# Kernel optimization log

Hardware: AMD Instinct MI355X
Metric: run time of the kernel (lower is better)

Reference implementation:

```python
import jax, jax.numpy as jnp
import numpy as np

B, S, D, H, DH = 2, 2048, 768, 12, 64
GAMMA = 0.5
SMOOTHING = 1.0  # softmax_attn_smoothing scalar (non-trainable weight in the original)
SCALE = 1.0 / float(np.sqrt(DH))


def setup_inputs() -> dict:
    key = jax.random.key(0)
    ks = jax.random.split(key, 8)
    w = 0.02
    return {
        "inp": jax.random.normal(ks[0], (B, S, D), dtype=jnp.float32),
        "pos_emb": jax.random.normal(ks[1], (S, D), dtype=jnp.float32),
        "Wq_inp": jax.random.normal(ks[2], (D, H * DH), dtype=jnp.float32) * w,
        "Wk_inp": jax.random.normal(ks[3], (D, H * DH), dtype=jnp.float32) * w,
        "Wq_pos": jax.random.normal(ks[4], (D, H * DH), dtype=jnp.float32) * w,
        "Wk_pos": jax.random.normal(ks[5], (D, H * DH), dtype=jnp.float32) * w,
        "Wv": jax.random.normal(ks[6], (D, H * DH), dtype=jnp.float32) * w,
        "Wo": jax.random.normal(ks[7], (H * DH, D), dtype=jnp.float32) * w,
    }


def reference(inp, pos_emb, Wq_inp, Wk_inp, Wq_pos, Wk_pos, Wv, Wo):
    # projections; note original reshape order: [..., d_head, n_head]
    q_i = (inp @ Wq_inp).reshape(B, S, DH, H)
    k_i = (inp @ Wk_inp).reshape(B, S, DH, H)
    q_p = (pos_emb @ Wq_pos).reshape(S, DH, H)
    k_p = (pos_emb @ Wk_pos).reshape(S, DH, H)
    v = (inp @ Wv).reshape(B, S, DH, H)

    # content-content stream: [B,S,S,H], softmax over key axis (axis=2)
    score_inp = jnp.einsum("bidh,bjdh->bijh", q_i, k_i) * (SCALE * SMOOTHING)
    prob_inp = jax.nn.softmax(score_inp, axis=2)

    # position-position stream: [S,S,H], softmax over key axis (axis=1)
    score_pos = jnp.einsum("idh,jdh->ijh", q_p, k_p) * (SCALE * SMOOTHING)
    prob_pos = jax.nn.softmax(score_pos, axis=1)[None]  # [1,S,S,H]

    # gamma blend of the two attention distributions
    attn_prob = (1.0 - GAMMA) * prob_inp + GAMMA * prob_pos  # [B,S,S,H]

    # V-weighted sum, merge heads as [..., h, d] per the original 'bihd' output
    attn_out = jnp.einsum("bijh,bjdh->bihd", attn_prob, v).reshape(B, S, H * DH)
    attn_out = attn_out @ Wo  # [B,S,D]
    return attn_out, attn_prob
```

## Files before the change

### kernel.cpp

```cpp
#include <hip/hip_runtime.h>
#include <hip/hip_bf16.h>

constexpr int NH  = 12;
constexpr int SEQ = 2048;
constexpr int DHD = 64;
constexpr int DIM = 768;
constexpr float QSCALE = 0.125f * 1.44269504088896f;

typedef __bf16 bf16x8 __attribute__((ext_vector_type(8)));
typedef __bf16 bf16x4 __attribute__((ext_vector_type(4)));
typedef float  f32x4  __attribute__((ext_vector_type(4)));

#define MFMA16(a, b, c) __builtin_amdgcn_mfma_f32_16x16x32_bf16((a), (b), (c), 0, 0, 0)

__global__ __launch_bounds__(256) void prep_kernel(
    const float* __restrict__ inp, const float* __restrict__ pos,
    const float* __restrict__ Wqi, const float* __restrict__ Wki,
    const float* __restrict__ Wvv, const float* __restrict__ Wqp,
    const float* __restrict__ Wkp,
    __bf16* __restrict__ Ab, __bf16* __restrict__ Pb, __bf16* __restrict__ Wp)
{
    const int bidx = blockIdx.x;
    const int tid = threadIdx.x;

    if (bidx < 2304) {
        const int idx = bidx * 256 + tid;
        constexpr int N8I = 4096 * 768 / 8;
        constexpr int N8P = 2048 * 768 / 8;
        if (idx >= N8I + N8P) return;
        const float* src; __bf16* dst; int off;
        if (idx < N8I) { src = inp; dst = Ab; off = idx; }
        else           { src = pos; dst = Pb; off = idx - N8I; }
        const float4 v0 = *reinterpret_cast<const float4*>(&src[(size_t)off * 8]);
        const float4 v1 = *reinterpret_cast<const float4*>(&src[(size_t)off * 8 + 4]);
        bf16x8 t;
        t[0] = (__bf16)v0.x; t[1] = (__bf16)v0.y; t[2] = (__bf16)v0.z; t[3] = (__bf16)v0.w;
        t[4] = (__bf16)v1.x; t[5] = (__bf16)v1.y; t[6] = (__bf16)v1.z; t[7] = (__bf16)v1.w;
        *reinterpret_cast<bf16x8*>(&dst[(size_t)off * 8]) = t;
        return;
    }

    const int pidx = bidx - 2304;
    const int kt = pidx % 12;
    const int h  = (pidx / 12) % 12;
    const int z  = pidx / 144;
    const int k0 = kt * 64;
    const float* W; float scale = 1.0f;
    if (z == 0)      { W = Wqi; scale = QSCALE; }
    else if (z == 1) { W = Wki; }
    else if (z == 2) { W = Wvv; }
    else if (z == 3) { W = Wqp; scale = QSCALE; }
    else             { W = Wkp; }

    __shared__ __bf16 lds[64][68];
    {
        const int d = tid & 63, kq = tid >> 6;
        #pragma unroll
        for (int rep = 0; rep < 16; ++rep) {
            const int kk = rep * 4 + kq;
            lds[kk][d] = (__bf16)(W[(size_t)(k0 + kk) * DIM + d * 12 + h] * scale);
        }
    }
    __syncthreads();
    {
        const int k = tid & 63, dq = tid >> 6;
        const size_t slab = ((size_t)z * 12 + h) * 64;
        #pragma unroll
        for (int rep = 0; rep < 16; ++rep) {
            const int d = rep * 4 + dq;
            Wp[(slab + d) * DIM + k0 + k] = lds[k][d];
        }
    }
}

__global__ __launch_bounds__(256) void proj_kernel(
    const __bf16* __restrict__ Ab, const __bf16* __restrict__ Pb,
    const __bf16* __restrict__ Wp,
    __bf16* __restrict__ Qi, __bf16* __restrict__ Ki, __bf16* __restrict__ Vsd,
    __bf16* __restrict__ Qp, __bf16* __restrict__ Kp)
{
    const int bx = blockIdx.x, h = blockIdx.y, z = blockIdx.z;
    if (z >= 3 && bx >= 8) return;
    const int tid = threadIdx.x, lane = tid & 63, wv = tid >> 6;
    const int l15 = lane & 15, lg = lane >> 4;
    const int m_w = bx * 256 + wv * 64;

    const __bf16* Asrc = (z < 3) ? Ab : Pb;
    const __bf16* Wsl = Wp + ((size_t)z * 12 + h) * 64 * DIM;

    f32x4 acc[4][4] = {};

    for (int kt = 0; kt < 24; ++kt) {
        const int k0 = kt * 32;
        bf16x8 a[4], b[4];
        #pragma unroll
        for (int mf = 0; mf < 4; ++mf)
            a[mf] = *reinterpret_cast<const bf16x8*>(
                &Asrc[(size_t)(m_w + mf * 16 + l15) * DIM + k0 + lg * 8]);
        #pragma unroll
        for (int nf = 0; nf < 4; ++nf)
            b[nf] = *reinterpret_cast<const bf16x8*>(
                &Wsl[(size_t)(nf * 16 + l15) * DIM + k0 + lg * 8]);
        #pragma unroll
        for (int mf = 0; mf < 4; ++mf)
            #pragma unroll
            for (int nf = 0; nf < 4; ++nf)
                acc[mf][nf] = MFMA16(a[mf], b[nf], acc[mf][nf]);
    }

    __bf16* outp = (z == 0) ? Qi : (z == 1) ? Ki : (z == 2) ? Vsd : (z == 3) ? Qp : Kp;
    #pragma unroll
    for (int mf = 0; mf < 4; ++mf)
        #pragma unroll
        for (int r = 0; r < 4; ++r) {
            const int m = m_w + mf * 16 + lg * 4 + r;
            const int s = m & 2047;
            const int slab = (z < 3) ? ((m >> 11) * 12 + h) : h;
            const size_t base = ((size_t)slab * SEQ + s) * DHD;
            #pragma unroll
            for (int nf = 0; nf < 4; ++nf)
                outp[base + nf * 16 + l15] = (__bf16)acc[mf][nf][r];
        }
}

__global__ __launch_bounds__(256) void vtrans_kernel(
    const __bf16* __restrict__ Vsd, __bf16* __restrict__ Vt)
{
    const int s0 = blockIdx.x * 64, slab = blockIdx.y;
    __shared__ __bf16 lds[64][66];
    const int tid = threadIdx.x;
    {
        const int rr = tid >> 3, cq = tid & 7;
        #pragma unroll
        for (int rep = 0; rep < 2; ++rep) {
            const int r2 = rr + rep * 32;
            *reinterpret_cast<bf16x8*>(&lds[r2][cq * 8]) =
                *reinterpret_cast<const bf16x8*>(
                    &Vsd[((size_t)slab * SEQ + s0 + r2) * DHD + cq * 8]);
        }
    }
    __syncthreads();
    {
        const int dd = tid >> 3, sq = tid & 7;
        #pragma unroll
        for (int rep = 0; rep < 2; ++rep) {
            const int d2 = dd + rep * 32;
            bf16x8 v;
            #pragma unroll
            for (int q = 0; q < 8; ++q) v[q] = lds[sq * 8 + q][d2];
            *reinterpret_cast<bf16x8*>(&Vt[((size_t)slab * DHD + d2) * SEQ + s0 + sq * 8]) = v;
        }
    }
}

__global__ __launch_bounds__(64) void stats_kernel(
    const __bf16* __restrict__ Qi, const __bf16* __restrict__ Ki,
    const __bf16* __restrict__ Qp, const __bf16* __restrict__ Kp,
    float* __restrict__ l_ws)
{
    const int bid = blockIdx.x + 128 * (blockIdx.y + 12 * blockIdx.z);
    const int wg = (bid & 7) * 576 + (bid >> 3);
    const int bx = wg & 127, h = (wg >> 7) % 12, bb = wg / 1536;

    const int lane = threadIdx.x;
    const int l15 = lane & 15, lg = lane >> 4;
    const int i0 = bx * 16;

    const __bf16* Q = (bb < 2) ? Qi + ((size_t)bb * NH + h) * SEQ * DHD
                               : Qp + (size_t)h * SEQ * DHD;
    const __bf16* K = (bb < 2) ? Ki + ((size_t)bb * NH + h) * SEQ * DHD
                               : Kp + (size_t)h * SEQ * DHD;

    bf16x8 a[2];
    #pragma unroll
    for (int ks = 0; ks < 2; ++ks)
        a[ks] = *reinterpret_cast<const bf16x8*>(
            &Q[(size_t)(i0 + l15) * DHD + ks * 32 + lg * 8]);

    float lr[4] = {};

    for (int jt = 0; jt < 32; ++jt) {
        const int j0 = jt * 64;
        bf16x8 bk[2][4];
        #pragma unroll
        for (int ks = 0; ks < 2; ++ks)
            #pragma unroll
            for (int nf = 0; nf < 4; ++nf)
                bk[ks][nf] = *reinterpret_cast<const bf16x8*>(
                    &K[(size_t)(j0 + nf * 16 + l15) * DHD + ks * 32 + lg * 8]);
        f32x4 c[4] = {};
        #pragma unroll
        for (int ks = 0; ks < 2; ++ks)
            #pragma unroll
            for (int nf = 0; nf < 4; ++nf)
                c[nf] = MFMA16(a[ks], bk[ks][nf], c[nf]);

        #pragma unroll
        for (int r = 0; r < 4; ++r)
            lr[r] += exp2f(c[0][r]) + exp2f(c[1][r])
                   + exp2f(c[2][r]) + exp2f(c[3][r]);
    }

    #pragma unroll
    for (int msk = 1; msk < 16; msk <<= 1)
        #pragma unroll
        for (int r = 0; r < 4; ++r)
            lr[r] += __shfl_xor(lr[r], msk);

    if (l15 == 0) {
        const size_t base = ((size_t)bb * NH + h) * SEQ + i0;
        #pragma unroll
        for (int r = 0; r < 4; ++r)
            l_ws[base + lg * 4 + r] = lr[r];
    }
}

__global__ __launch_bounds__(384) void emit_kernel(
    const __bf16* __restrict__ Qi, const __bf16* __restrict__ Ki,
    const __bf16* __restrict__ Qp, const __bf16* __restrict__ Kp,
    const __bf16* __restrict__ Vt,
    const float* __restrict__ l_ws,
    float* __restrict__ out1, float* __restrict__ attn_pre)
{
    const int bid = blockIdx.x + 128 * (blockIdx.y + 4 * blockIdx.z);
    const int wg = (bid & 7) * 128 + (bid >> 3);
    const int it = wg & 127, js = (wg >> 7) & 3, b = wg >> 9;

    const int i0 = it * 16;
    const int tid = threadIdx.x, lane = tid & 63, wv = tid >> 6;
    const int l15 = lane & 15, lg = lane >> 4;

    __shared__ __align__(16) __bf16 ppv[12][16][40];
    __shared__ __align__(16) __bf16 pb2[2][16][32][12];
    __shared__ float ml[12][16][2];
    const __bf16* p2flat = &pb2[0][0][0][0];

    if (tid < 192) {
        const int h = tid >> 4, i = tid & 15;
        ml[h][i][0] = 0.5f / l_ws[((size_t)b * NH + h) * SEQ + i0 + i];
        ml[h][i][1] = 0.5f / l_ws[((size_t)2 * NH + h) * SEQ + i0 + i];
    }
    __syncthreads();

    const __bf16* Kb[2][2];
    bf16x8 aQ[2][2][2];
    #pragma unroll
    for (int hh = 0; hh < 2; ++hh) {
        const int h = wv * 2 + hh;
        Kb[hh][0] = Ki + ((size_t)b * NH + h) * SEQ * DHD;
        Kb[hh][1] = Kp + (size_t)h * SEQ * DHD;
        #pragma unroll
        for (int ks = 0; ks < 2; ++ks) {
            aQ[hh][0][ks] = *reinterpret_cast<const bf16x8*>(
                &Qi[(((size_t)b * NH + h) * SEQ + i0 + l15) * DHD + ks * 32 + lg * 8]);
            aQ[hh][1][ks] = *reinterpret_cast<const bf16x8*>(
                &Qp[((size_t)h * SEQ + i0 + l15) * DHD + ks * 32 + lg * 8]);
        }
    }

    bf16x8 kf[2][2][2][2];
    {
        const int j0 = js * 512;
        #pragma unroll
        for (int hh = 0; hh < 2; ++hh)
            #pragma unroll
            for (int st = 0; st < 2; ++st)
                #pragma unroll
                for (int nf = 0; nf < 2; ++nf)
                    #pragma unroll
                    for (int ks = 0; ks < 2; ++ks)
                        kf[hh][st][nf][ks] = *reinterpret_cast<const bf16x8*>(
                            &Kb[hh][st][(size_t)(j0 + nf * 16 + l15) * DHD + ks * 32 + lg * 8]);
    }

    f32x4 acc[2][4] = {};

    #pragma unroll 1
    for (int jt = 0; jt < 16; ++jt) {
        const int j0 = js * 512 + jt * 32;
        const int jn = (js * 512 + (jt + 1) * 32) & (SEQ - 1);
        const int buf = jt & 1;

        f32x4 ci[2][2] = {}, cq[2][2] = {};
        #pragma unroll
        for (int hh = 0; hh < 2; ++hh)
            #pragma unroll
            for (int ks = 0; ks < 2; ++ks)
                #pragma unroll
                for (int nf = 0; nf < 2; ++nf) {
                    ci[hh][nf] = MFMA16(aQ[hh][0][ks], kf[hh][0][nf][ks], ci[hh][nf]);
                    cq[hh][nf] = MFMA16(aQ[hh][1][ks], kf[hh][1][nf][ks], cq[hh][nf]);
                }

        #pragma unroll
        for (int hh = 0; hh < 2; ++hh)
            #pragma unroll
            for (int st = 0; st < 2; ++st)
                #pragma unroll
                for (int nf = 0; nf < 2; ++nf)
                    #pragma unroll
                    for (int ks = 0; ks < 2; ++ks)
                        kf[hh][st][nf][ks] = *reinterpret_cast<const bf16x8*>(
                            &Kb[hh][st][(size_t)(jn + nf * 16 + l15) * DHD + ks * 32 + lg * 8]);

        #pragma unroll
        for (int hh = 0; hh < 2; ++hh) {
            const int h = wv * 2 + hh;
            #pragma unroll
            for (int r = 0; r < 4; ++r) {
                const int i = lg * 4 + r;
                const float s0 = ml[h][i][0], s1 = ml[h][i][1];
                #pragma unroll
                for (int nf = 0; nf < 2; ++nf) {
                    const float pi_ = exp2f(ci[hh][nf][r]) * s0;
                    const float pq_ = exp2f(cq[hh][nf][r]) * s1;
                    const __bf16 p = (__bf16)(pi_ + pq_);
                    const int jj = nf * 16 + l15;
                    ppv[h][i][jj] = p;
                    pb2[buf][i][jj][h] = p;
                }
            }
        }

        #pragma unroll
        for (int hh = 0; hh < 2; ++hh) {
            const int h = wv * 2 + hh;
            const bf16x8 ap = *reinterpret_cast<const bf16x8*>(&ppv[h][l15][lg * 8]);
            #pragma unroll
            for (int nf = 0; nf < 4; ++nf) {
                const bf16x8 bv = *reinterpret_cast<const bf16x8*>(
                    &Vt[(((size_t)b * NH + h) * DHD + nf * 16 + l15) * SEQ + j0 + lg * 8]);
                acc[hh][nf] = MFMA16(ap, bv, acc[hh][nf]);
            }
        }
        __syncthreads();

        #pragma unroll
        for (int k = 0; k < 4; ++k) {
            const int o = (wv * 4 + k) * 256 + 4 * lane;
            const int i = o / 384;
            const int rem = o - i * 384;
            const bf16x4 pv4 = *reinterpret_cast<const bf16x4*>(&p2flat[buf * 6144 + o]);
            f32x4 v;
            #pragma unroll
            for (int q = 0; q < 4; ++q) v[q] = (float)pv4[q];
            const size_t addr = ((size_t)(b * SEQ + i0 + i) * SEQ + j0) * 12 + rem;
            *reinterpret_cast<f32x4*>(&out1[addr]) = v;
        }
    }

    #pragma unroll
    for (int hh = 0; hh < 2; ++hh) {
        const int h = wv * 2 + hh;
        #pragma unroll
        for (int nf = 0; nf < 4; ++nf)
            #pragma unroll
            for (int r = 0; r < 4; ++r) {
                const int i = lg * 4 + r;
                atomicAdd(&attn_pre[((size_t)(b * SEQ + i0 + i)) * DIM + h * DHD + nf * 16 + l15],
                          acc[hh][nf][r]);
            }
    }
}

__global__ __launch_bounds__(256) void final_kernel(
    const float* __restrict__ A, const float* __restrict__ W, float* __restrict__ out0)
{
    const int m0 = blockIdx.y * 64;
    const int n0 = blockIdx.x * 192;

    __shared__ __bf16 Al[64][32];
    __shared__ __bf16 Wl[192][32];

    const int tid = threadIdx.x;
    const int lane = tid & 63, wv = tid >> 6;
    const int wm = wv >> 1, wn = wv & 1;
    const int l15 = lane & 15, lg = lane >> 4;

    f32x4 c[2][6] = {};

    for (int kt = 0; kt < 24; ++kt) {
        const int k0 = kt * 32;
        __syncthreads();
        {
            const int r = tid >> 3, kq = tid & 7;
            #pragma unroll
            for (int rep = 0; rep < 2; ++rep) {
                const float4 v = *reinterpret_cast<const float4*>(
                    &A[(size_t)(m0 + r + rep * 32) * DIM + k0 + kq * 4]);
                bf16x4 t;
                t[0] = (__bf16)v.x; t[1] = (__bf16)v.y; t[2] = (__bf16)v.z; t[3] = (__bf16)v.w;
                *reinterpret_cast<bf16x4*>(&Al[r + rep * 32][kq * 4]) = t;
            }
        }
        for (int idx = tid; idx < 32 * 48; idx += 256) {
            const int k = idx / 48, nq = idx - k * 48;
            const float4 v = *reinterpret_cast<const float4*>(
                &W[(size_t)(k0 + k) * DIM + n0 + nq * 4]);
            Wl[nq * 4 + 0][k] = (__bf16)v.x;
            Wl[nq * 4 + 1][k] = (__bf16)v.y;
            Wl[nq * 4 + 2][k] = (__bf16)v.z;
            Wl[nq * 4 + 3][k] = (__bf16)v.w;
        }
        __syncthreads();

        bf16x8 a[2], b[6];
        #pragma unroll
        for (int mf = 0; mf < 2; ++mf)
            a[mf] = *reinterpret_cast<const bf16x8*>(&Al[wm * 32 + mf * 16 + l15][lg * 8]);
        #pragma unroll
        for (int nf = 0; nf < 6; ++nf)
            b[nf] = *reinterpret_cast<const bf16x8*>(&Wl[wn * 96 + nf * 16 + l15][lg * 8]);
        #pragma unroll
        for (int mf = 0; mf < 2; ++mf)
            #pragma unroll
            for (int nf = 0; nf < 6; ++nf)
                c[mf][nf] = MFMA16(a[mf], b[nf], c[mf][nf]);
    }

    #pragma unroll
    for (int mf = 0; mf < 2; ++mf)
        #pragma unroll
        for (int nf = 0; nf < 6; ++nf)
            #pragma unroll
            for (int r = 0; r < 4; ++r) {
                const int m = m0 + wm * 32 + mf * 16 + lg * 4 + r;
                const int n = n0 + wn * 96 + nf * 16 + l15;
                out0[(size_t)m * DIM + n] = c[mf][nf][r];
            }
}

extern "C" void kernel_launch(void* const* d_in, const int* in_sizes, int n_in,
                              void* d_out, int out_size, void* d_ws, size_t ws_size,
                              hipStream_t stream)
{
    (void)in_sizes; (void)n_in; (void)out_size; (void)ws_size;

    const float* inp = (const float*)d_in[0];
    const float* pos = (const float*)d_in[1];
    const float* Wqi = (const float*)d_in[2];
    const float* Wki = (const float*)d_in[3];
    const float* Wqp = (const float*)d_in[4];
    const float* Wkp = (const float*)d_in[5];
    const float* Wvv = (const float*)d_in[6];
    const float* Wo  = (const float*)d_in[7];

    char* w = (char*)d_ws;
    __bf16* Ab = (__bf16*)w;  w += (size_t)4096 * 768 * 2;
    __bf16* Pb = (__bf16*)w;  w += (size_t)2048 * 768 * 2;
    __bf16* Wp = (__bf16*)w;  w += (size_t)5 * 768 * 768 * 2;
    __bf16* Qi = (__bf16*)w;  w += (size_t)2 * NH * SEQ * DHD * 2;
    __bf16* Ki = (__bf16*)w;  w += (size_t)2 * NH * SEQ * DHD * 2;
    __bf16* Vsd = (__bf16*)w; w += (size_t)2 * NH * SEQ * DHD * 2;
    __bf16* Qp = (__bf16*)w;  w += (size_t)NH * SEQ * DHD * 2;
    __bf16* Kp = (__bf16*)w;  w += (size_t)NH * SEQ * DHD * 2;
    float* l_ws = (float*)w;  w += (size_t)3 * NH * SEQ * 4;
    float* attn_pre = (float*)w; w += (size_t)4096 * DIM * 4;
    __bf16* Vt = Ab;

    float* out0 = (float*)d_out;
    float* out1 = out0 + (size_t)2 * SEQ * DIM;

    hipMemsetAsync(attn_pre, 0, (size_t)4096 * DIM * 4, stream);

    hipLaunchKernelGGL(prep_kernel, dim3(3024), dim3(256), 0, stream,
                       inp, pos, Wqi, Wki, Wvv, Wqp, Wkp, Ab, Pb, Wp);
    hipLaunchKernelGGL(proj_kernel, dim3(16, 12, 5), dim3(256), 0, stream,
                       Ab, Pb, Wp, Qi, Ki, Vsd, Qp, Kp);
    hipLaunchKernelGGL(vtrans_kernel, dim3(32, 24), dim3(256), 0, stream, Vsd, Vt);
    hipLaunchKernelGGL(stats_kernel, dim3(128, 12, 3), dim3(64), 0, stream,
                       Qi, Ki, Qp, Kp, l_ws);
    hipLaunchKernelGGL(emit_kernel, dim3(128, 4, 2), dim3(384), 0, stream,
                       Qi, Ki, Qp, Kp, Vt, l_ws, out1, attn_pre);
    hipLaunchKernelGGL(final_kernel, dim3(4, 64, 1), dim3(256), 0, stream,
                       attn_pre, Wo, out0);
}
```

Baseline: 688.2 us.

## Merge stats and V-transpose kernels, pack P LDS writes, widen attn_prob stores

Fuses the softmax-denominator stats kernel and the V transpose into one launch, interleaving block roles 3:2 over a 1920-block grid, with stats blocks grown to four waves of 16 rows each. In the emit kernel, the two heads' bf16 probabilities are packed into a single 32-bit LDS write, and the fp32 attn_prob output copy uses 8-element reads with two 16-byte stores per lane. The aim is to save a launch and its tail, cut LDS store instructions, and widen global stores on the large attn_prob output. The mixed-role grid brings divergent block durations and shared-memory allocation on stats blocks that do not use it.

New measurement: 685.3 us, median of 3. No clear change (-0.4%).

```diff
diff --git a/kernel.cpp b/kernel.cpp
--- a/kernel.cpp
+++ b/kernel.cpp
@@ -123,12 +123,77 @@
         }
 }
 
-__global__ __launch_bounds__(256) void vtrans_kernel(
-    const __bf16* __restrict__ Vsd, __bf16* __restrict__ Vt)
-{
-    const int s0 = blockIdx.x * 64, slab = blockIdx.y;
+__global__ __launch_bounds__(256) void sv_kernel(
+    const __bf16* __restrict__ Qi, const __bf16* __restrict__ Ki,
+    const __bf16* __restrict__ Qp, const __bf16* __restrict__ Kp,
+    const __bf16* __restrict__ Vsd,
+    float* __restrict__ l_ws, __bf16* __restrict__ Vt)
+{
+    const int bid = blockIdx.x;
+    const int m5 = bid % 5;
+    const int tid = threadIdx.x;
+
     __shared__ __bf16 lds[64][66];
-    const int tid = threadIdx.x;
+
+    if (m5 < 3) {
+        const int si = (bid / 5) * 3 + m5;
+        const int bx = si & 31, h = (si >> 5) % 12, bb = si / 384;
+        const int lane = tid & 63, wv = tid >> 6;
+        const int l15 = lane & 15, lg = lane >> 4;
+        const int i0 = bx * 64 + wv * 16;
+
+        const __bf16* Q = (bb < 2) ? Qi + ((size_t)bb * NH + h) * SEQ * DHD
+                                   : Qp + (size_t)h * SEQ * DHD;
+        const __bf16* K = (bb < 2) ? Ki + ((size_t)bb * NH + h) * SEQ * DHD
+                                   : Kp + (size_t)h * SEQ * DHD;
+
+        bf16x8 a[2];
+        #pragma unroll
+        for (int ks = 0; ks < 2; ++ks)
+            a[ks] = *reinterpret_cast<const bf16x8*>(
+                &Q[(size_t)(i0 + l15) * DHD + ks * 32 + lg * 8]);
+
+        float lr[4] = {};
+
+        for (int jt = 0; jt < 32; ++jt) {
+            const int j0 = jt * 64;
+            bf16x8 bk[2][4];
+            #pragma unroll
+            for (int ks = 0; ks < 2; ++ks)
+                #pragma unroll
+                for (int nf = 0; nf < 4; ++nf)
+                    bk[ks][nf] = *reinterpret_cast<const bf16x8*>(
+                        &K[(size_t)(j0 + nf * 16 + l15) * DHD + ks * 32 + lg * 8]);
+            f32x4 c[4] = {};
+            #pragma unroll
+            for (int ks = 0; ks < 2; ++ks)
+                #pragma unroll
+                for (int nf = 0; nf < 4; ++nf)
+                    c[nf] = MFMA16(a[ks], bk[ks][nf], c[nf]);
+
+            #pragma unroll
+            for (int r = 0; r < 4; ++r)
+                lr[r] += exp2f(c[0][r]) + exp2f(c[1][r])
+                       + exp2f(c[2][r]) + exp2f(c[3][r]);
+        }
+
+        #pragma unroll
+        for (int msk = 1; msk < 16; msk <<= 1)
+            #pragma unroll
+            for (int r = 0; r < 4; ++r)
+                lr[r] += __shfl_xor(lr[r], msk);
+
+        if (l15 == 0) {
+            const size_t base = ((size_t)bb * NH + h) * SEQ + i0;
+            #pragma unroll
+            for (int r = 0; r < 4; ++r)
+                l_ws[base + lg * 4 + r] = lr[r];
+        }
+        return;
+    }
+
+    const int vi = (bid / 5) * 2 + (m5 - 3);
+    const int s0 = (vi & 31) * 64, slab = vi >> 5;
     {
         const int rr = tid >> 3, cq = tid & 7;
         #pragma unroll
@@ -150,68 +215,6 @@
             for (int q = 0; q < 8; ++q) v[q] = lds[sq * 8 + q][d2];
             *reinterpret_cast<bf16x8*>(&Vt[((size_t)slab * DHD + d2) * SEQ + s0 + sq * 8]) = v;
         }
-    }
-}
-
-__global__ __launch_bounds__(64) void stats_kernel(
-    const __bf16* __restrict__ Qi, const __bf16* __restrict__ Ki,
-    const __bf16* __restrict__ Qp, const __bf16* __restrict__ Kp,
-    float* __restrict__ l_ws)
-{
-    const int bid = blockIdx.x + 128 * (blockIdx.y + 12 * blockIdx.z);
-    const int wg = (bid & 7) * 576 + (bid >> 3);
-    const int bx = wg & 127, h = (wg >> 7) % 12, bb = wg / 1536;
-
-    const int lane = threadIdx.x;
-    const int l15 = lane & 15, lg = lane >> 4;
-    const int i0 = bx * 16;
-
-    const __bf16* Q = (bb < 2) ? Qi + ((size_t)bb * NH + h) * SEQ * DHD
-                               : Qp + (size_t)h * SEQ * DHD;
-    const __bf16* K = (bb < 2) ? Ki + ((size_t)bb * NH + h) * SEQ * DHD
-                               : Kp + (size_t)h * SEQ * DHD;
-
-    bf16x8 a[2];
-    #pragma unroll
-    for (int ks = 0; ks < 2; ++ks)
-        a[ks] = *reinterpret_cast<const bf16x8*>(
-            &Q[(size_t)(i0 + l15) * DHD + ks * 32 + lg * 8]);
-
-    float lr[4] = {};
-
-    for (int jt = 0; jt < 32; ++jt) {
-        const int j0 = jt * 64;
-        bf16x8 bk[2][4];
-        #pragma unroll
-        for (int ks = 0; ks < 2; ++ks)
-            #pragma unroll
-            for (int nf = 0; nf < 4; ++nf)
-                bk[ks][nf] = *reinterpret_cast<const bf16x8*>(
-                    &K[(size_t)(j0 + nf * 16 + l15) * DHD + ks * 32 + lg * 8]);
-        f32x4 c[4] = {};
-        #pragma unroll
-        for (int ks = 0; ks < 2; ++ks)
-            #pragma unroll
-            for (int nf = 0; nf < 4; ++nf)
-                c[nf] = MFMA16(a[ks], bk[ks][nf], c[nf]);
-
-        #pragma unroll
-        for (int r = 0; r < 4; ++r)
-            lr[r] += exp2f(c[0][r]) + exp2f(c[1][r])
-                   + exp2f(c[2][r]) + exp2f(c[3][r]);
-    }
-
-    #pragma unroll
-    for (int msk = 1; msk < 16; msk <<= 1)
-        #pragma unroll
-        for (int r = 0; r < 4; ++r)
-            lr[r] += __shfl_xor(lr[r], msk);
-
-    if (l15 == 0) {
-        const size_t base = ((size_t)bb * NH + h) * SEQ + i0;
-        #pragma unroll
-        for (int r = 0; r < 4; ++r)
-            l_ws[base + lg * 4 + r] = lr[r];
     }
 }
 
@@ -304,21 +307,22 @@
                             &Kb[hh][st][(size_t)(jn + nf * 16 + l15) * DHD + ks * 32 + lg * 8]);
 
         #pragma unroll
-        for (int hh = 0; hh < 2; ++hh) {
-            const int h = wv * 2 + hh;
-            #pragma unroll
-            for (int r = 0; r < 4; ++r) {
-                const int i = lg * 4 + r;
-                const float s0 = ml[h][i][0], s1 = ml[h][i][1];
-                #pragma unroll
-                for (int nf = 0; nf < 2; ++nf) {
-                    const float pi_ = exp2f(ci[hh][nf][r]) * s0;
-                    const float pq_ = exp2f(cq[hh][nf][r]) * s1;
+        for (int r = 0; r < 4; ++r) {
+            const int i = lg * 4 + r;
+            #pragma unroll
+            for (int nf = 0; nf < 2; ++nf) {
+                const int jj = nf * 16 + l15;
+                union { __bf16 h2[2]; unsigned u; } uu;
+                #pragma unroll
+                for (int hh = 0; hh < 2; ++hh) {
+                    const int h = wv * 2 + hh;
+                    const float pi_ = exp2f(ci[hh][nf][r]) * ml[h][i][0];
+                    const float pq_ = exp2f(cq[hh][nf][r]) * ml[h][i][1];
                     const __bf16 p = (__bf16)(pi_ + pq_);
-                    const int jj = nf * 16 + l15;
                     ppv[h][i][jj] = p;
-                    pb2[buf][i][jj][h] = p;
+                    uu.h2[hh] = p;
                 }
+                *reinterpret_cast<unsigned*>(&pb2[buf][i][jj][wv * 2]) = uu.u;
             }
         }
 
@@ -336,16 +340,17 @@
         __syncthreads();
 
         #pragma unroll
-        for (int k = 0; k < 4; ++k) {
-            const int o = (wv * 4 + k) * 256 + 4 * lane;
+        for (int kk = 0; kk < 2; ++kk) {
+            const int o = (wv * 2 + kk) * 512 + 8 * lane;
             const int i = o / 384;
             const int rem = o - i * 384;
-            const bf16x4 pv4 = *reinterpret_cast<const bf16x4*>(&p2flat[buf * 6144 + o]);
-            f32x4 v;
-            #pragma unroll
-            for (int q = 0; q < 4; ++q) v[q] = (float)pv4[q];
+            const bf16x8 pv8 = *reinterpret_cast<const bf16x8*>(&p2flat[buf * 6144 + o]);
+            f32x4 v0, v1;
+            #pragma unroll
+            for (int q = 0; q < 4; ++q) { v0[q] = (float)pv8[q]; v1[q] = (float)pv8[4 + q]; }
             const size_t addr = ((size_t)(b * SEQ + i0 + i) * SEQ + j0) * 12 + rem;
-            *reinterpret_cast<f32x4*>(&out1[addr]) = v;
+            *reinterpret_cast<f32x4*>(&out1[addr])     = v0;
+            *reinterpret_cast<f32x4*>(&out1[addr + 4]) = v1;
         }
     }
 
@@ -467,9 +472,8 @@
                        inp, pos, Wqi, Wki, Wvv, Wqp, Wkp, Ab, Pb, Wp);
     hipLaunchKernelGGL(proj_kernel, dim3(16, 12, 5), dim3(256), 0, stream,
                        Ab, Pb, Wp, Qi, Ki, Vsd, Qp, Kp);
-    hipLaunchKernelGGL(vtrans_kernel, dim3(32, 24), dim3(256), 0, stream, Vsd, Vt);
-    hipLaunchKernelGGL(stats_kernel, dim3(128, 12, 3), dim3(64), 0, stream,
-                       Qi, Ki, Qp, Kp, l_ws);
+    hipLaunchKernelGGL(sv_kernel, dim3(1920), dim3(256), 0, stream,
+                       Qi, Ki, Qp, Kp, Vsd, l_ws, Vt);
     hipLaunchKernelGGL(emit_kernel, dim3(128, 4, 2), dim3(384), 0, stream,
                        Qi, Ki, Qp, Kp, Vt, l_ws, out1, attn_pre);
     hipLaunchKernelGGL(final_kernel, dim3(4, 64, 1), dim3(256), 0, stream,
```
